# Kernel tuning notes

Measured on AMD Instinct MI355X. Metric: run time of the kernel, lower is better.

## Reference

```python
import jax, jax.numpy as jnp
import numpy as np

T, N, F = 8, 128, 128


def setup_inputs() -> dict:
    key = jax.random.key(0)
    k1, k2, k3, k4 = jax.random.split(key, 4)
    node_feats = jax.random.normal(k1, (T, N, F), dtype=jnp.float32)
    edge_feats = jax.random.normal(k2, (T, N, N, F), dtype=jnp.float32)
    # Conv3d(in=3, out=1, kernel=1) weights flattened to 3 scalars + bias
    w = jax.random.normal(k3, (3,), dtype=jnp.float32)
    b = jax.random.normal(k4, (1,), dtype=jnp.float32)
    return {"node_feats": node_feats, "edge_feats": edge_feats, "w": w, "b": b}


def reference(node_feats, edge_feats, w, b):
    # node_feats: [T, N, F]; edge_feats: [T, N, N, F]
    x_i = node_feats[:, :, None, :]          # [T, N, 1, F] -> broadcast over j
    x_ij = x_i - node_feats[:, None, :, :]    # [T, N, N, F]  (x_i - x_j)
    # fused 1x1x1 conv over the 3 stacked channels + bias, then tanh
    e = jnp.tanh(w[0] * x_i + w[1] * x_ij + w[2] * edge_feats + b[0])  # [T, N, N, F]
    n = e.shape[1]
    diag_mask = (1.0 - jnp.eye(n, dtype=e.dtype))[None, :, :, None]
    e = e * diag_mask
    # original returns transpose(1,3) of [T,F,i,j] -> [T,j,i,F]: swap i and j
    return jnp.swapaxes(e, 1, 2)
```

## Files before the change

### kernel.cpp

```cpp
#include <hip/hip_runtime.h>


typedef float f32x4 __attribute__((ext_vector_type(4)));

__device__ __forceinline__ float fast_tanh(float x) {
    x = fminf(fmaxf(x, -9.0f), 9.0f);
    float t = __expf(2.0f * x);
    return (t - 1.0f) / (t + 1.0f);
}

__global__ __launch_bounds__(256)
void EdgeUpdateNetwork_44555990729422_kernel(
    const float* __restrict__ node,
    const float* __restrict__ edge,
    const float* __restrict__ w,
    const float* __restrict__ b,
    float* __restrict__ out)
{
    __shared__ f32x4 tile[8 * 8 * 32];

    const float w1  = w[1];
    const float w01 = w[0] + w1;
    const float w2  = w[2];
    const float bb  = b[0];

    const int blk = blockIdx.x;
    const int jb  = blk & 15;
    const int ib  = (blk >> 4) & 15;
    const int t   = blk >> 8;
    const int i0  = ib << 3;
    const int j0  = jb << 3;

    const int tid = threadIdx.x;
    const int f4  = tid & 31;
    const int dq  = tid >> 5;

    const f32x4* __restrict__ node4 = reinterpret_cast<const f32x4*>(node);
    const f32x4* __restrict__ edge4 = reinterpret_cast<const f32x4*>(edge);
    f32x4* __restrict__ out4        = reinterpret_cast<f32x4*>(out);

    f32x4 nj = node4[((t << 7) + j0 + dq) * 32 + f4];
    const float cx = fmaf(-w1, nj.x, bb);
    const float cy = fmaf(-w1, nj.y, bb);
    const float cz = fmaf(-w1, nj.z, bb);
    const float cw = fmaf(-w1, nj.w, bb);

    #pragma unroll
    for (int r = 0; r < 8; ++r) {
        const int i = i0 + r;
        f32x4 ni = node4[((t << 7) + i) * 32 + f4];
        f32x4 e  = edge4[(((t << 7) + i) * 128 + j0 + dq) * 32 + f4];
        const float m = (i == j0 + dq) ? 0.0f : 1.0f;
        f32x4 rv;
        rv.x = m * fast_tanh(fmaf(w01, ni.x, fmaf(w2, e.x, cx)));
        rv.y = m * fast_tanh(fmaf(w01, ni.y, fmaf(w2, e.y, cy)));
        rv.z = m * fast_tanh(fmaf(w01, ni.z, fmaf(w2, e.z, cz)));
        rv.w = m * fast_tanh(fmaf(w01, ni.w, fmaf(w2, e.w, cw)));
        tile[(dq * 8 + r) * 32 + f4] = rv;
    }

    __syncthreads();

    #pragma unroll
    for (int r = 0; r < 8; ++r) {
        f32x4 v = tile[(r * 8 + dq) * 32 + f4];
        const int j = j0 + r;
        __builtin_nontemporal_store(
            v, &out4[(((t << 7) + j) * 128 + i0 + dq) * 32 + f4]);
    }
}

extern "C" void kernel_launch(void* const* d_in, const int* in_sizes, int n_in,
                              void* d_out, int out_size, void* d_ws, size_t ws_size,
                              hipStream_t stream) {
    const float* node = (const float*)d_in[0];
    const float* edge = (const float*)d_in[1];
    const float* w    = (const float*)d_in[2];
    const float* b    = (const float*)d_in[3];
    float* out        = (float*)d_out;

    EdgeUpdateNetwork_44555990729422_kernel<<<2048, 256, 0, stream>>>(
        node, edge, w, b, out);
}
```

Baseline: 26.23 us.

## Replace shared-memory transpose with intra-wave shuffle and smaller i-tiles

Drops the LDS tile and __syncthreads used to swap the i and j axes. Each wave now handles two j rows, and the 2x2 transpose is done with a cross-half-wave shuffle. The block tile shrinks to 4 i by 8 j, so the grid doubles to 4096 blocks, and an occupancy hint is added to launch bounds. This removes LDS traffic and the barrier, at the cost of shuffle instructions and shorter contiguous store runs per wave.

```diff
diff --git a/kernel.cpp b/kernel.cpp
--- a/kernel.cpp
+++ b/kernel.cpp
@@ -9,7 +9,16 @@
     return (t - 1.0f) / (t + 1.0f);
 }
 
-__global__ __launch_bounds__(256)
+__device__ __forceinline__ f32x4 shfl_xor32(f32x4 v) {
+    f32x4 r;
+    r.x = __shfl_xor(v.x, 32, 64);
+    r.y = __shfl_xor(v.y, 32, 64);
+    r.z = __shfl_xor(v.z, 32, 64);
+    r.w = __shfl_xor(v.w, 32, 64);
+    return r;
+}
+
+__global__ __launch_bounds__(256, 8)
 void EdgeUpdateNetwork_44555990729422_kernel(
     const float* __restrict__ node,
     const float* __restrict__ edge,
@@ -17,8 +26,6 @@
     const float* __restrict__ b,
     float* __restrict__ out)
 {
-    __shared__ f32x4 tile[8 * 8 * 32];
-
     const float w1  = w[1];
     const float w01 = w[0] + w1;
     const float w2  = w[2];
@@ -26,47 +33,50 @@
 
     const int blk = blockIdx.x;
     const int jb  = blk & 15;
-    const int ib  = (blk >> 4) & 15;
-    const int t   = blk >> 8;
-    const int i0  = ib << 3;
+    const int ib  = (blk >> 4) & 31;
+    const int t   = blk >> 9;
+    const int i0  = ib << 2;
     const int j0  = jb << 3;
 
-    const int tid = threadIdx.x;
-    const int f4  = tid & 31;
-    const int dq  = tid >> 5;
+    const int tid  = threadIdx.x;
+    const int wv   = tid >> 6;
+    const int lane = tid & 63;
+    const int dq   = lane >> 5;
+    const int f4   = lane & 31;
+
+    const int jp = j0 + (wv << 1);
+    const int jl = jp + dq;
 
     const f32x4* __restrict__ node4 = reinterpret_cast<const f32x4*>(node);
     const f32x4* __restrict__ edge4 = reinterpret_cast<const f32x4*>(edge);
     f32x4* __restrict__ out4        = reinterpret_cast<f32x4*>(out);
 
-    f32x4 nj = node4[((t << 7) + j0 + dq) * 32 + f4];
-    const float cx = fmaf(-w1, nj.x, bb);
-    const float cy = fmaf(-w1, nj.y, bb);
-    const float cz = fmaf(-w1, nj.z, bb);
-    const float cw = fmaf(-w1, nj.w, bb);
+    f32x4 nj = node4[(t * 128 + jl) * 32 + f4];
+    f32x4 c  = (-w1) * nj + bb;
+
+    f32x4 rv[4];
+    #pragma unroll
+    for (int r = 0; r < 4; ++r) {
+        const int i = i0 + r;
+        f32x4 ni = node4[(t * 128 + i) * 32 + f4];
+        f32x4 e  = edge4[((t * 128 + i) * 128 + jl) * 32 + f4];
+        f32x4 x  = w01 * ni + w2 * e + c;
+        const float m = (i == jl) ? 0.0f : 1.0f;
+        rv[r].x = m * fast_tanh(x.x);
+        rv[r].y = m * fast_tanh(x.y);
+        rv[r].z = m * fast_tanh(x.z);
+        rv[r].w = m * fast_tanh(x.w);
+    }
 
     #pragma unroll
-    for (int r = 0; r < 8; ++r) {
-        const int i = i0 + r;
-        f32x4 ni = node4[((t << 7) + i) * 32 + f4];
-        f32x4 e  = edge4[(((t << 7) + i) * 128 + j0 + dq) * 32 + f4];
-        const float m = (i == j0 + dq) ? 0.0f : 1.0f;
-        f32x4 rv;
-        rv.x = m * fast_tanh(fmaf(w01, ni.x, fmaf(w2, e.x, cx)));
-        rv.y = m * fast_tanh(fmaf(w01, ni.y, fmaf(w2, e.y, cy)));
-        rv.z = m * fast_tanh(fmaf(w01, ni.z, fmaf(w2, e.z, cz)));
-        rv.w = m * fast_tanh(fmaf(w01, ni.w, fmaf(w2, e.w, cw)));
-        tile[(dq * 8 + r) * 32 + f4] = rv;
-    }
-
-    __syncthreads();
-
-    #pragma unroll
-    for (int r = 0; r < 8; ++r) {
-        f32x4 v = tile[(r * 8 + dq) * 32 + f4];
-        const int j = j0 + r;
-        __builtin_nontemporal_store(
-            v, &out4[(((t << 7) + j) * 128 + i0 + dq) * 32 + f4]);
+    for (int s = 0; s < 2; ++s) {
+        const int iw = i0 + (s << 1) + dq;
+        f32x4 send = (dq == 0) ? rv[2 * s + 1] : rv[2 * s];
+        f32x4 recv = shfl_xor32(send);
+        f32x4 v0 = (dq == 0) ? rv[2 * s] : recv;
+        f32x4 v1 = (dq == 0) ? recv : rv[2 * s + 1];
+        __builtin_nontemporal_store(v0, &out4[((t * 128 + jp    ) * 128 + iw) * 32 + f4]);
+        __builtin_nontemporal_store(v1, &out4[((t * 128 + jp + 1) * 128 + iw) * 32 + f4]);
     }
 }
 
@@ -79,6 +89,6 @@
     const float* b    = (const float*)d_in[3];
     float* out        = (float*)d_out;
 
-    EdgeUpdateNetwork_44555990729422_kernel<<<2048, 256, 0, stream>>>(
+    EdgeUpdateNetwork_44555990729422_kernel<<<4096, 256, 0, stream>>>(
         node, edge, w, b, out);
 }
```

Measured after the change: 25.35 us. 3.4% less time.
